# Optimization experiments

Hardware: AMD Instinct MI355X
Metric: run time of the kernel (lower is better)

## Reference

```python
import jax, jax.numpy as jnp
import numpy as np

B, NODES, IN_DIM, OUT_DIM, CAPS, K, NUM_ROUTE = 32, 512, 256, 128, 16, 5, 3

def squash(s):
    # s: [..., out]; scale = |s|^2/(1+|s|^2), direction s/(|s|+eps)
    sn = jnp.sum(s * s, axis=-1, keepdims=True)
    return (sn / (1.0 + sn)) * s / (jnp.sqrt(sn) + 1e-8)

def setup_inputs() -> dict:
    key = jax.random.key(0)
    k1, k2, k3, k4 = jax.random.split(key, 4)
    return {
        "x": jax.random.normal(k1, (B, NODES, IN_DIM), jnp.float32),
        "contribution": jax.random.normal(k2, (B, NODES), jnp.float32),
        "W": jax.random.normal(k3, (K, IN_DIM, OUT_DIM), jnp.float32),
        "alpha": jax.random.normal(k4, (NODES, CAPS, K), jnp.float32),
    }

def reference(x, contribution, W, alpha):
    # per-node, per-capsule transform: sum_k alpha[n,c,k] * W[k,i,o] -> [nodes, caps, in, out]
    Wn = jnp.einsum('nck,kio->ncio', alpha, W)
    # prediction vectors u_hat: [B, caps, nodes, out]
    u_hat = jnp.einsum('bni,ncio->bcno', x, Wn)
    u_det = jax.lax.stop_gradient(u_hat)
    # routing logits b init from (detached) contribution: [B, caps, nodes, 1]
    b = jnp.broadcast_to(
        jax.lax.stop_gradient(contribution)[:, None, :, None],
        (x.shape[0], CAPS, x.shape[1], 1))
    for _ in range(NUM_ROUTE):
        c = jax.nn.softmax(b, axis=1)              # over capsule axis
        v = squash(jnp.sum(c * u_det, axis=2))     # [B, caps, out]
        b = b + jnp.einsum('bcno,bco->bcn', u_det, v)[..., None]
    c = jax.nn.softmax(b, axis=1)
    s = jnp.sum(c * u_hat, axis=2)                 # [B, caps, out] (non-detached)
    return squash(s)
```

## Files before the change

### kernel.cpp

```cpp
#include <hip/hip_runtime.h>
#include <math.h>

#define B_ 32
#define NODES_ 512
#define IN_ 256
#define OUT_ 128
#define CAPS_ 16
#define KW_ 5
#define M_ (B_*NODES_)
#define N_ (KW_*OUT_)
#define NCH 32

typedef __attribute__((ext_vector_type(8))) short short8;
typedef __attribute__((ext_vector_type(4))) float f32x4;

#define Y_BOFF   0
#define L_BOFF   41943040
#define V_BOFF   42991616
#define SP_BOFF  43253760
#define BT_SZ    (N_*IN_*2)

__device__ __forceinline__ float b2f(unsigned short u) {
  union { unsigned int i; float f; } c; c.i = ((unsigned int)u) << 16; return c.f;
}
__device__ __forceinline__ unsigned short f2b(float f) {
  union { float f; unsigned int i; } c; c.f = f;
  unsigned int u = c.i;
  u += 0x7fffu + ((u >> 16) & 1u);
  return (unsigned short)(u >> 16);
}
__device__ __forceinline__ void async_load16(const void* g, void* l) {
  __builtin_amdgcn_global_load_lds(
      (const __attribute__((address_space(1))) unsigned int*)g,
      (__attribute__((address_space(3))) unsigned int*)l, 16, 0, 0);
}

__global__ __launch_bounds__(256) void conv_w(const float* __restrict__ W,
                                              unsigned short* __restrict__ bThi,
                                              unsigned short* __restrict__ bTlo) {
  int n = blockIdx.x;
  int i = threadIdx.x;
  int k = n >> 7, o = n & 127;
  float v = W[((size_t)k*IN_ + i)*OUT_ + o];
  unsigned short h = f2b(v);
  size_t dst = ((size_t)(i >> 3)*N_ + n)*8 + (i & 7);
  bThi[dst] = h;
  bTlo[dst] = f2b(v - b2f(h));
}

__global__ __launch_bounds__(512) void gemm_fn(const float* __restrict__ x,
                                               const unsigned short* __restrict__ bThi,
                                               const unsigned short* __restrict__ bTlo,
                                               float* __restrict__ y) {
  __shared__ float A_lds[8*64*4];
  __shared__ short Bh_lds[4*640*8];
  __shared__ short Bl_lds[4*640*8];
  const int t    = threadIdx.x;
  const int w    = t >> 6;
  const int lane = t & 63;
  const int lrow = lane & 15;
  const int lk   = lane >> 4;
  const int m0   = blockIdx.x * 64;
  const int wn0  = w * 80;
  const int arow = t >> 3;
  const int ac4  = t & 7;

  f32x4 acc[4][5];
  #pragma unroll
  for (int i=0;i<4;++i)
    #pragma unroll
    for (int j=0;j<5;++j) acc[i][j] = (f32x4){0.f,0.f,0.f,0.f};

  for (int kbi = 0; kbi < 8; ++kbi) {
    const int kb = kbi*32;
    const unsigned short* bh_src = bThi + (size_t)kbi*4*N_*8;
    const unsigned short* bl_src = bTlo + (size_t)kbi*4*N_*8;
    #pragma unroll
    for (int q=0; q<5; ++q) {
      int db = q*512 + w*64;
      async_load16(bh_src + (size_t)(db + lane)*8, &Bh_lds[db*8]);
      async_load16(bl_src + (size_t)(db + lane)*8, &Bl_lds[db*8]);
    }
    {
      float4 av = *(const float4*)(x + (size_t)(m0 + arow)*IN_ + kb + ac4*4);
      *(float4*)&A_lds[((ac4*64) + arow)*4] = av;
    }
    __syncthreads();

    short8 ah[4], al[4];
    #pragma unroll
    for (int mi=0; mi<4; ++mi) {
      int row = mi*16 + lrow;
      f32x4 a0 = *(const f32x4*)&A_lds[((2*lk  )*64 + row)*4];
      f32x4 a1 = *(const f32x4*)&A_lds[((2*lk+1)*64 + row)*4];
      #pragma unroll
      for (int j=0; j<8; ++j) {
        float f = (j < 4) ? a0[j] : a1[j-4];
        unsigned short h = f2b(f);
        ah[mi][j] = (short)h;
        al[mi][j] = (short)f2b(f - b2f(h));
      }
    }
    #pragma unroll
    for (int ni=0; ni<5; ++ni) {
      int nb = wn0 + ni*16 + lrow;
      short8 bh = *(const short8*)&Bh_lds[(lk*N_ + nb)*8];
      short8 bl = *(const short8*)&Bl_lds[(lk*N_ + nb)*8];
      #pragma unroll
      for (int mi=0; mi<4; ++mi) {
        acc[mi][ni] = __builtin_amdgcn_mfma_f32_16x16x32_bf16(bh, ah[mi], acc[mi][ni], 0, 0, 0);
        acc[mi][ni] = __builtin_amdgcn_mfma_f32_16x16x32_bf16(bh, al[mi], acc[mi][ni], 0, 0, 0);
        acc[mi][ni] = __builtin_amdgcn_mfma_f32_16x16x32_bf16(bl, ah[mi], acc[mi][ni], 0, 0, 0);
      }
    }
    __syncthreads();
  }

  #pragma unroll
  for (int mi=0; mi<4; ++mi) {
    int m = m0 + mi*16 + lrow;
    #pragma unroll
    for (int ni=0; ni<5; ++ni) {
      int nb = wn0 + ni*16 + lk*4;
      float4 o = {acc[mi][ni][0], acc[mi][ni][1], acc[mi][ni][2], acc[mi][ni][3]};
      *(float4*)(y + (size_t)m*N_ + nb) = o;
    }
  }
}

__global__ __launch_bounds__(512) void route512(const float* __restrict__ y,
                                                const float* __restrict__ alpha,
                                                const float* __restrict__ contrib,
                                                float* __restrict__ logits,
                                                const float* __restrict__ vin,
                                                float* __restrict__ s_part,
                                                int mode) {
  __shared__ __align__(16) float sh_y[16*640];
  __shared__ __align__(16) float sh_v[16*132];
  __shared__ __align__(16) float sh_alpha[16*16*5];
  __shared__ float sh_logit[16][16];

  const int t  = threadIdx.x;
  const int ch = blockIdx.x;
  const int b  = blockIdx.y;
  const int n0 = ch*16;
  const int node1 = t >> 5;
  const int cap1  = (t >> 1) & 15;
  const int half  = t & 1;

  const float* ybase = y + ((size_t)(b*NODES_ + n0))*N_;
  #pragma unroll
  for (int q=0; q<5; ++q) {
    int d0 = q*512 + (t & ~63);
    async_load16(ybase + (size_t)(d0 + (t & 63))*4, &sh_y[d0*4]);
  }
  const float* abase = alpha + (size_t)n0*CAPS_*KW_;
  if (t < 320) {
    float4 av = *(const float4*)(abase + t*4);
    *(float4*)&sh_alpha[t*4] = av;
  }
  float lreg = 0.f;
  if (mode >= 1) {
    int flat = t*4;
    float4 vv = *(const float4*)(vin + (size_t)b*CAPS_*OUT_ + flat);
    *(float4*)&sh_v[(flat >> 7)*132 + (flat & 127)] = vv;
    lreg = logits[((size_t)b*CAPS_ + cap1)*NODES_ + n0 + node1];
  } else {
    if (t < 256) {
      int nd = t >> 4, cp = t & 15;
      logits[((size_t)b*CAPS_ + cp)*NODES_ + n0 + nd] =
          contrib[(size_t)b*NODES_ + n0 + nd];
    }
  }
  __syncthreads();

  if (mode >= 1) {
    const float* al = &sh_alpha[(node1*16+cap1)*5];
    float a0=al[0],a1=al[1],a2=al[2],a3=al[3],a4=al[4];
    const float* yb = &sh_y[node1*640] + half*64;
    const float* vb = &sh_v[cap1*132]  + half*64;
    float accd = 0.f;
    #pragma unroll 4
    for (int o=0; o<64; o+=4) {
      float4 y0 = *(const float4*)(yb + 0*128 + o);
      float4 y1 = *(const float4*)(yb + 1*128 + o);
      float4 y2 = *(const float4*)(yb + 2*128 + o);
      float4 y3 = *(const float4*)(yb + 3*128 + o);
      float4 y4 = *(const float4*)(yb + 4*128 + o);
      float4 vv = *(const float4*)(vb + o);
      float ux = a0*y0.x + a1*y1.x + a2*y2.x + a3*y3.x + a4*y4.x;
      float uy = a0*y0.y + a1*y1.y + a2*y2.y + a3*y3.y + a4*y4.y;
      float uz = a0*y0.z + a1*y1.z + a2*y2.z + a3*y3.z + a4*y4.z;
      float uw = a0*y0.w + a1*y1.w + a2*y2.w + a3*y3.w + a4*y4.w;
      accd += ux*vv.x + uy*vv.y + uz*vv.z + uw*vv.w;
    }
    float tot = accd + __shfl_xor(accd, 1, 64);
    float newl = lreg + tot;
    if (half == 0)
      logits[((size_t)b*CAPS_ + cap1)*NODES_ + n0 + node1] = newl;
    float m = newl;
    m = fmaxf(m, __shfl_xor(m, 2, 64));
    m = fmaxf(m, __shfl_xor(m, 4, 64));
    m = fmaxf(m, __shfl_xor(m, 8, 64));
    m = fmaxf(m, __shfl_xor(m, 16, 64));
    float e = __expf(newl - m);
    float ssum = e;
    ssum += __shfl_xor(ssum, 2, 64);
    ssum += __shfl_xor(ssum, 4, 64);
    ssum += __shfl_xor(ssum, 8, 64);
    ssum += __shfl_xor(ssum, 16, 64);
    if (half == 0) sh_logit[node1][cap1] = e / ssum;
  } else {
    if (t < 256) sh_logit[t >> 4][t & 15] = 0.0625f;
  }
  __syncthreads();

  {
    int c = t & 15;
    int o = (t >> 4) * 4;
    float4 acc = {0.f,0.f,0.f,0.f};
    #pragma unroll 4
    for (int nd=0; nd<16; ++nd) {
      const float* al2 = &sh_alpha[(nd*16+c)*5];
      float a0=al2[0],a1=al2[1],a2=al2[2],a3=al2[3],a4=al2[4];
      const float* yb2 = &sh_y[nd*640 + o];
      float4 y0 = *(const float4*)(yb2);
      float4 y1 = *(const float4*)(yb2 + 128);
      float4 y2 = *(const float4*)(yb2 + 256);
      float4 y3 = *(const float4*)(yb2 + 384);
      float4 y4 = *(const float4*)(yb2 + 512);
      float cw = sh_logit[nd][c];
      acc.x += cw*(a0*y0.x + a1*y1.x + a2*y2.x + a3*y3.x + a4*y4.x);
      acc.y += cw*(a0*y0.y + a1*y1.y + a2*y2.y + a3*y3.y + a4*y4.y);
      acc.z += cw*(a0*y0.z + a1*y1.z + a2*y2.z + a3*y3.z + a4*y4.z);
      acc.w += cw*(a0*y0.w + a1*y1.w + a2*y2.w + a3*y3.w + a4*y4.w);
    }
    *(float4*)(s_part + ((size_t)(b*NCH + ch)*CAPS_ + c)*OUT_ + o) = acc;
  }
}

__global__ __launch_bounds__(128) void squash_k(const float* __restrict__ s_part,
                                                float* __restrict__ out) {
  const int bc = blockIdx.x;
  const int o  = threadIdx.x;
  const int b = bc >> 4, c = bc & 15;
  const float* sp = s_part + ((size_t)(b*NCH)*CAPS_ + c)*OUT_ + o;
  float s = 0.f;
  #pragma unroll
  for (int ch=0; ch<NCH; ++ch) s += sp[(size_t)ch*CAPS_*OUT_];
  float ss = s*s;
  #pragma unroll
  for (int off=32; off>0; off>>=1) ss += __shfl_down(ss, off, 64);
  __shared__ float red[2];
  if ((o & 63) == 0) red[o>>6] = ss;
  __syncthreads();
  float sn = red[0] + red[1];
  float scale = (sn/(1.f+sn)) / (sqrtf(sn)+1e-8f);
  out[(size_t)bc*OUT_ + o] = scale*s;
}

extern "C" void kernel_launch(void* const* d_in, const int* in_sizes, int n_in,
                              void* d_out, int out_size, void* d_ws, size_t ws_size,
                              hipStream_t stream) {
  const float* x       = (const float*)d_in[0];
  const float* contrib = (const float*)d_in[1];
  const float* W       = (const float*)d_in[2];
  const float* alpha   = (const float*)d_in[3];
  float* out = (float*)d_out;
  char*  wsb = (char*)d_ws;

  float* y             = (float*)(wsb + Y_BOFF);
  float* logits        = (float*)(wsb + L_BOFF);
  float* v             = (float*)(wsb + V_BOFF);
  float* s_part        = (float*)(wsb + SP_BOFF);
  unsigned short* bThi = (unsigned short*)(wsb + SP_BOFF);
  unsigned short* bTlo = (unsigned short*)(wsb + SP_BOFF + BT_SZ);

  conv_w<<<N_, 256, 0, stream>>>(W, bThi, bTlo);
  gemm_fn<<<M_/64, 512, 0, stream>>>(x, bThi, bTlo, y);

  route512<<<dim3(NCH, B_), 512, 0, stream>>>(y, alpha, contrib, logits, v, s_part, 0);
  squash_k<<<B_*CAPS_, 128, 0, stream>>>(s_part, v);

  for (int it=0; it<3; ++it) {
    route512<<<dim3(NCH, B_), 512, 0, stream>>>(y, alpha, contrib, logits, v, s_part, 1);
    squash_k<<<B_*CAPS_, 128, 0, stream>>>(s_part, (it==2) ? out : v);
  }
}
```

Measured before the change: 153.3 us.

## Fuse routing iterations and squash into one persistent kernel with per-batch barriers

Replaces the eight alternating route and squash launches with a single kernel of 512 blocks. Each batch's 16 blocks loop over all routing iterations and synchronise through atomic-counter barriers, and logits now stay in registers instead of round-tripping through global memory. The aim is to remove launch overhead and inter-kernel gaps. In exchange, each block now handles two node chunks with 256 threads, so it reloads y from global every iteration. The spin barriers also assume all 16 blocks of a batch are co-resident, which risks deadlock or stalls if they are not.

```diff
diff --git a/kernel.cpp b/kernel.cpp
--- a/kernel.cpp
+++ b/kernel.cpp
@@ -15,7 +15,7 @@
 typedef __attribute__((ext_vector_type(4))) float f32x4;
 
 #define Y_BOFF   0
-#define L_BOFF   41943040
+#define CTR_BOFF 41943040
 #define V_BOFF   42991616
 #define SP_BOFF  43253760
 #define BT_SZ    (N_*IN_*2)
@@ -33,6 +33,17 @@
   __builtin_amdgcn_global_load_lds(
       (const __attribute__((address_space(1))) unsigned int*)g,
       (__attribute__((address_space(3))) unsigned int*)l, 16, 0, 0);
+}
+
+__device__ __forceinline__ void batch_bar(int* c) {
+  __syncthreads();
+  if (threadIdx.x == 0) {
+    __threadfence();
+    atomicAdd(c, 1);
+    while (atomicAdd(c, 0) < 16) {}
+  }
+  __syncthreads();
+  __threadfence();
 }
 
 __global__ __launch_bounds__(256) void conv_w(const float* __restrict__ W,
@@ -128,135 +139,157 @@
   }
 }
 
-__global__ __launch_bounds__(512) void route512(const float* __restrict__ y,
-                                                const float* __restrict__ alpha,
-                                                const float* __restrict__ contrib,
-                                                float* __restrict__ logits,
-                                                const float* __restrict__ vin,
-                                                float* __restrict__ s_part,
-                                                int mode) {
+__global__ __launch_bounds__(256) void route_batch(const float* __restrict__ y,
+                                                   const float* __restrict__ alpha,
+                                                   const float* __restrict__ contrib,
+                                                   float* __restrict__ v,
+                                                   float* __restrict__ s_part,
+                                                   float* __restrict__ out,
+                                                   int* __restrict__ ctr) {
   __shared__ __align__(16) float sh_y[16*640];
   __shared__ __align__(16) float sh_v[16*132];
   __shared__ __align__(16) float sh_alpha[16*16*5];
   __shared__ float sh_logit[16][16];
-
-  const int t  = threadIdx.x;
-  const int ch = blockIdx.x;
-  const int b  = blockIdx.y;
-  const int n0 = ch*16;
-  const int node1 = t >> 5;
-  const int cap1  = (t >> 1) & 15;
-  const int half  = t & 1;
-
-  const float* ybase = y + ((size_t)(b*NODES_ + n0))*N_;
+  __shared__ float sh_red[256];
+  __shared__ float sh_ss[2];
+
+  const int t    = threadIdx.x;
+  const int bx   = blockIdx.x;
+  const int b    = bx >> 4;
+  const int cp   = bx & 15;
+  const int node = t >> 4, cap = t & 15;
+  int* bctr = ctr + b*8;
+
+  float lreg[2];
   #pragma unroll
-  for (int q=0; q<5; ++q) {
-    int d0 = q*512 + (t & ~63);
-    async_load16(ybase + (size_t)(d0 + (t & 63))*4, &sh_y[d0*4]);
+  for (int hh=0; hh<2; ++hh)
+    lreg[hh] = contrib[(size_t)b*NODES_ + (cp*2+hh)*16 + node];
+
+  for (int it = 0; it < 4; ++it) {
+    if (it >= 1) {
+      const float* vbase = v + (size_t)b*CAPS_*OUT_;
+      #pragma unroll
+      for (int q=0; q<2; ++q) {
+        int flat = (t + q*256)*4;
+        int c = flat >> 7, o = flat & 127;
+        float4 vv = *(const float4*)(vbase + flat);
+        *(float4*)&sh_v[c*132 + o] = vv;
+      }
+    }
+
+    #pragma unroll
+    for (int hh=0; hh<2; ++hh) {
+      const int ch = cp*2 + hh;
+      const int n0 = ch*16;
+
+      const float* ybase = y + ((size_t)(b*NODES_ + n0))*N_;
+      #pragma unroll
+      for (int q=0; q<10; ++q) {
+        int d0 = q*256 + (t & ~63);
+        async_load16(ybase + (size_t)(d0 + (t & 63))*4, &sh_y[d0*4]);
+      }
+      const float* abase = alpha + (size_t)n0*CAPS_*KW_;
+      for (int i = t; i < 320; i += 256) {
+        float4 av = *(const float4*)(abase + i*4);
+        *(float4*)&sh_alpha[i*4] = av;
+      }
+      __syncthreads();
+
+      if (it >= 1) {
+        const float* al = &sh_alpha[(node*16+cap)*5];
+        float a0=al[0],a1=al[1],a2=al[2],a3=al[3],a4=al[4];
+        const float* yb = &sh_y[node*640];
+        const float* vb = &sh_v[cap*132];
+        float accd = 0.f;
+        #pragma unroll 4
+        for (int o=0; o<128; o+=4) {
+          float4 y0 = *(const float4*)(yb + 0*128 + o);
+          float4 y1 = *(const float4*)(yb + 1*128 + o);
+          float4 y2 = *(const float4*)(yb + 2*128 + o);
+          float4 y3 = *(const float4*)(yb + 3*128 + o);
+          float4 y4 = *(const float4*)(yb + 4*128 + o);
+          float4 vv = *(const float4*)(vb + o);
+          float ux = a0*y0.x + a1*y1.x + a2*y2.x + a3*y3.x + a4*y4.x;
+          float uy = a0*y0.y + a1*y1.y + a2*y2.y + a3*y3.y + a4*y4.y;
+          float uz = a0*y0.z + a1*y1.z + a2*y2.z + a3*y3.z + a4*y4.z;
+          float uw = a0*y0.w + a1*y1.w + a2*y2.w + a3*y3.w + a4*y4.w;
+          accd += ux*vv.x + uy*vv.y + uz*vv.z + uw*vv.w;
+        }
+        float newl = lreg[hh] + accd;
+        lreg[hh] = newl;
+        float m = newl;
+        m = fmaxf(m, __shfl_xor(m, 1, 64));
+        m = fmaxf(m, __shfl_xor(m, 2, 64));
+        m = fmaxf(m, __shfl_xor(m, 4, 64));
+        m = fmaxf(m, __shfl_xor(m, 8, 64));
+        float e = __expf(newl - m);
+        float ssum = e;
+        ssum += __shfl_xor(ssum, 1, 64);
+        ssum += __shfl_xor(ssum, 2, 64);
+        ssum += __shfl_xor(ssum, 4, 64);
+        ssum += __shfl_xor(ssum, 8, 64);
+        sh_logit[node][cap] = e / ssum;
+      } else {
+        sh_logit[node][cap] = 0.0625f;
+      }
+      __syncthreads();
+
+      float* spb = s_part + ((size_t)(b*NCH + ch))*CAPS_*OUT_;
+      #pragma unroll
+      for (int sl=0; sl<2; ++sl) {
+        int slot = t + sl*256;
+        int c  = slot & 15;
+        int o  = (slot >> 4) * 4;
+        float4 acc = {0.f,0.f,0.f,0.f};
+        #pragma unroll 4
+        for (int nd=0; nd<16; ++nd) {
+          const float* al2 = &sh_alpha[(nd*16+c)*5];
+          float a0=al2[0],a1=al2[1],a2=al2[2],a3=al2[3],a4=al2[4];
+          const float* yb2 = &sh_y[nd*640 + o];
+          float4 y0 = *(const float4*)(yb2);
+          float4 y1 = *(const float4*)(yb2 + 128);
+          float4 y2 = *(const float4*)(yb2 + 256);
+          float4 y3 = *(const float4*)(yb2 + 384);
+          float4 y4 = *(const float4*)(yb2 + 512);
+          float cw = sh_logit[nd][c];
+          acc.x += cw*(a0*y0.x + a1*y1.x + a2*y2.x + a3*y3.x + a4*y4.x);
+          acc.y += cw*(a0*y0.y + a1*y1.y + a2*y2.y + a3*y3.y + a4*y4.y);
+          acc.z += cw*(a0*y0.z + a1*y1.z + a2*y2.z + a3*y3.z + a4*y4.z);
+          acc.w += cw*(a0*y0.w + a1*y1.w + a2*y2.w + a3*y3.w + a4*y4.w);
+        }
+        *(float4*)(spb + c*OUT_ + o) = acc;
+      }
+      __syncthreads();
+    }
+
+    batch_bar(&bctr[it*2]);
+
+    {
+      const int o = t & 127, h = t >> 7;
+      const float* sp = s_part + ((size_t)(b*NCH + h*16)*CAPS_ + cp)*OUT_ + o;
+      float part = 0.f;
+      #pragma unroll
+      for (int cc=0; cc<16; ++cc) part += sp[(size_t)cc*CAPS_*OUT_];
+      sh_red[h*128 + o] = part;
+      __syncthreads();
+      float s = 0.f;
+      if (t < 128) {
+        s = sh_red[t] + sh_red[128 + t];
+        float ss = s*s;
+        #pragma unroll
+        for (int off=32; off>0; off>>=1) ss += __shfl_down(ss, off, 64);
+        if ((t & 63) == 0) sh_ss[t>>6] = ss;
+      }
+      __syncthreads();
+      if (t < 128) {
+        float sn = sh_ss[0] + sh_ss[1];
+        float scale = (sn/(1.f+sn)) / (sqrtf(sn)+1e-8f);
+        float* dst = (it==3) ? out : v;
+        dst[((size_t)b*CAPS_ + cp)*OUT_ + t] = scale*s;
+      }
+    }
+    if (it < 3) batch_bar(&bctr[it*2+1]);
   }
-  const float* abase = alpha + (size_t)n0*CAPS_*KW_;
-  if (t < 320) {
-    float4 av = *(const float4*)(abase + t*4);
-    *(float4*)&sh_alpha[t*4] = av;
-  }
-  float lreg = 0.f;
-  if (mode >= 1) {
-    int flat = t*4;
-    float4 vv = *(const float4*)(vin + (size_t)b*CAPS_*OUT_ + flat);
-    *(float4*)&sh_v[(flat >> 7)*132 + (flat & 127)] = vv;
-    lreg = logits[((size_t)b*CAPS_ + cap1)*NODES_ + n0 + node1];
-  } else {
-    if (t < 256) {
-      int nd = t >> 4, cp = t & 15;
-      logits[((size_t)b*CAPS_ + cp)*NODES_ + n0 + nd] =
-          contrib[(size_t)b*NODES_ + n0 + nd];
-    }
-  }
-  __syncthreads();
-
-  if (mode >= 1) {
-    const float* al = &sh_alpha[(node1*16+cap1)*5];
-    float a0=al[0],a1=al[1],a2=al[2],a3=al[3],a4=al[4];
-    const float* yb = &sh_y[node1*640] + half*64;
-    const float* vb = &sh_v[cap1*132]  + half*64;
-    float accd = 0.f;
-    #pragma unroll 4
-    for (int o=0; o<64; o+=4) {
-      float4 y0 = *(const float4*)(yb + 0*128 + o);
-      float4 y1 = *(const float4*)(yb + 1*128 + o);
-      float4 y2 = *(const float4*)(yb + 2*128 + o);
-      float4 y3 = *(const float4*)(yb + 3*128 + o);
-      float4 y4 = *(const float4*)(yb + 4*128 + o);
-      float4 vv = *(const float4*)(vb + o);
-      float ux = a0*y0.x + a1*y1.x + a2*y2.x + a3*y3.x + a4*y4.x;
-      float uy = a0*y0.y + a1*y1.y + a2*y2.y + a3*y3.y + a4*y4.y;
-      float uz = a0*y0.z + a1*y1.z + a2*y2.z + a3*y3.z + a4*y4.z;
-      float uw = a0*y0.w + a1*y1.w + a2*y2.w + a3*y3.w + a4*y4.w;
-      accd += ux*vv.x + uy*vv.y + uz*vv.z + uw*vv.w;
-    }
-    float tot = accd + __shfl_xor(accd, 1, 64);
-    float newl = lreg + tot;
-    if (half == 0)
-      logits[((size_t)b*CAPS_ + cap1)*NODES_ + n0 + node1] = newl;
-    float m = newl;
-    m = fmaxf(m, __shfl_xor(m, 2, 64));
-    m = fmaxf(m, __shfl_xor(m, 4, 64));
-    m = fmaxf(m, __shfl_xor(m, 8, 64));
-    m = fmaxf(m, __shfl_xor(m, 16, 64));
-    float e = __expf(newl - m);
-    float ssum = e;
-    ssum += __shfl_xor(ssum, 2, 64);
-    ssum += __shfl_xor(ssum, 4, 64);
-    ssum += __shfl_xor(ssum, 8, 64);
-    ssum += __shfl_xor(ssum, 16, 64);
-    if (half == 0) sh_logit[node1][cap1] = e / ssum;
-  } else {
-    if (t < 256) sh_logit[t >> 4][t & 15] = 0.0625f;
-  }
-  __syncthreads();
-
-  {
-    int c = t & 15;
-    int o = (t >> 4) * 4;
-    float4 acc = {0.f,0.f,0.f,0.f};
-    #pragma unroll 4
-    for (int nd=0; nd<16; ++nd) {
-      const float* al2 = &sh_alpha[(nd*16+c)*5];
-      float a0=al2[0],a1=al2[1],a2=al2[2],a3=al2[3],a4=al2[4];
-      const float* yb2 = &sh_y[nd*640 + o];
-      float4 y0 = *(const float4*)(yb2);
-      float4 y1 = *(const float4*)(yb2 + 128);
-      float4 y2 = *(const float4*)(yb2 + 256);
-      float4 y3 = *(const float4*)(yb2 + 384);
-      float4 y4 = *(const float4*)(yb2 + 512);
-      float cw = sh_logit[nd][c];
-      acc.x += cw*(a0*y0.x + a1*y1.x + a2*y2.x + a3*y3.x + a4*y4.x);
-      acc.y += cw*(a0*y0.y + a1*y1.y + a2*y2.y + a3*y3.y + a4*y4.y);
-      acc.z += cw*(a0*y0.z + a1*y1.z + a2*y2.z + a3*y3.z + a4*y4.z);
-      acc.w += cw*(a0*y0.w + a1*y1.w + a2*y2.w + a3*y3.w + a4*y4.w);
-    }
-    *(float4*)(s_part + ((size_t)(b*NCH + ch)*CAPS_ + c)*OUT_ + o) = acc;
-  }
-}
-
-__global__ __launch_bounds__(128) void squash_k(const float* __restrict__ s_part,
-                                                float* __restrict__ out) {
-  const int bc = blockIdx.x;
-  const int o  = threadIdx.x;
-  const int b = bc >> 4, c = bc & 15;
-  const float* sp = s_part + ((size_t)(b*NCH)*CAPS_ + c)*OUT_ + o;
-  float s = 0.f;
-  #pragma unroll
-  for (int ch=0; ch<NCH; ++ch) s += sp[(size_t)ch*CAPS_*OUT_];
-  float ss = s*s;
-  #pragma unroll
-  for (int off=32; off>0; off>>=1) ss += __shfl_down(ss, off, 64);
-  __shared__ float red[2];
-  if ((o & 63) == 0) red[o>>6] = ss;
-  __syncthreads();
-  float sn = red[0] + red[1];
-  float scale = (sn/(1.f+sn)) / (sqrtf(sn)+1e-8f);
-  out[(size_t)bc*OUT_ + o] = scale*s;
 }
 
 extern "C" void kernel_launch(void* const* d_in, const int* in_sizes, int n_in,
@@ -270,7 +303,7 @@
   char*  wsb = (char*)d_ws;
 
   float* y             = (float*)(wsb + Y_BOFF);
-  float* logits        = (float*)(wsb + L_BOFF);
+  int*   ctr           = (int*)(wsb + CTR_BOFF);
   float* v             = (float*)(wsb + V_BOFF);
   float* s_part        = (float*)(wsb + SP_BOFF);
   unsigned short* bThi = (unsigned short*)(wsb + SP_BOFF);
@@ -279,11 +312,7 @@
   conv_w<<<N_, 256, 0, stream>>>(W, bThi, bTlo);
   gemm_fn<<<M_/64, 512, 0, stream>>>(x, bThi, bTlo, y);
 
-  route512<<<dim3(NCH, B_), 512, 0, stream>>>(y, alpha, contrib, logits, v, s_part, 0);
-  squash_k<<<B_*CAPS_, 128, 0, stream>>>(s_part, v);
-
-  for (int it=0; it<3; ++it) {
-    route512<<<dim3(NCH, B_), 512, 0, stream>>>(y, alpha, contrib, logits, v, s_part, 1);
-    squash_k<<<B_*CAPS_, 128, 0, stream>>>(s_part, (it==2) ? out : v);
-  }
-}
+  hipMemsetAsync(ctr, 0, 32*8*sizeof(int), stream);
+
+  route_batch<<<512, 256, 0, stream>>>(y, alpha, contrib, v, s_part, out, ctr);
+}
```

Result: slower. 525.1 us (+242.6%).
